# Performance work log

Hardware: AMD Instinct MI355X
Metric: run time of the kernel (lower is better)

Reference implementation:

```python
import jax, jax.numpy as jnp
import numpy as np

N, D, K = 500000, 256, 64

def setup_inputs() -> dict:
    key = jax.random.key(0)
    kq, km = jax.random.split(key)
    query = jax.random.normal(kq, (D,), dtype=jnp.float32)
    mat = jax.random.normal(km, (N, D), dtype=jnp.float32)
    return {"query": query, "mat": mat, "k": K}

def reference(query, mat, k):
    # scores = mat @ query  : [N]
    scores = jnp.einsum("nd,d->n", mat, query)
    # top-k selection over all stored vectors
    _, idx = jax.lax.top_k(scores, k)
    # gather the selected rows : [k, D]
    out = jnp.take(mat, idx, axis=0)
    # idx stands in for the metadata gather (meta[i] for i in idx)
    return out, idx
```

## Files before the change

kernel.cpp:

```cpp
#include <hip/hip_runtime.h>
#include <stdint.h>

#define DIM 256
#define TOPK 64
#define HIST_BINS 65536
#define CAP 4096

__device__ __forceinline__ uint32_t fkey(float f) {
  uint32_t u = __float_as_uint(f);
  return (u & 0x80000000u) ? ~u : (u | 0x80000000u);
}

__global__ __launch_bounds__(256) void score_kernel(
    const float* __restrict__ mat, const float* __restrict__ query,
    float* __restrict__ scores, uint32_t* __restrict__ hist,
    int* __restrict__ cnt, int n) {
  int tid = blockIdx.x * 256 + threadIdx.x;
  if (tid < HIST_BINS) hist[tid] = 0u;
  if (tid == 0) *cnt = 0;

  int wave = tid >> 6;
  int lane = threadIdx.x & 63;
  if (wave < n) {
    float4 q = ((const float4*)query)[lane];
    float4 m = ((const float4*)(mat + (size_t)wave * DIM))[lane];
    float d = m.x * q.x + m.y * q.y + m.z * q.z + m.w * q.w;
#pragma unroll
    for (int off = 32; off > 0; off >>= 1) d += __shfl_xor(d, off, 64);
    if (lane == 0) scores[wave] = d;
  }
}

__global__ __launch_bounds__(256) void hist_kernel(
    const float* __restrict__ scores, uint32_t* __restrict__ hist, int n) {
  int i = blockIdx.x * 256 + threadIdx.x;
  int stride = gridDim.x * 256;
  for (; i < n; i += stride) {
    atomicAdd(&hist[fkey(scores[i]) >> 16], 1u);
  }
}

__global__ __launch_bounds__(256) void thresh_kernel(
    const uint32_t* __restrict__ hist, int* __restrict__ tbin) {
  __shared__ uint32_t s[256];
  __shared__ int fc;
  __shared__ uint32_t above;
  int t = threadIdx.x;

  uint32_t acc = 0;
  const uint4* h4 = (const uint4*)(hist + t * 256);
  for (int j = 0; j < 64; ++j) {
    uint4 v = h4[j];
    acc += v.x + v.y + v.z + v.w;
  }
  s[t] = acc;
  __syncthreads();
  for (int off = 1; off < 256; off <<= 1) {
    uint32_t v = (t + off < 256) ? s[t + off] : 0u;
    __syncthreads();
    s[t] += v;
    __syncthreads();
  }
  if (s[t] >= TOPK && (t == 255 || s[t + 1] < TOPK)) {
    fc = t;
    above = (t == 255) ? 0u : s[t + 1];
  }
  __syncthreads();
  int c = fc;
  uint32_t a = above;
  uint32_t h = hist[c * 256 + t];
  __syncthreads();
  s[t] = h;
  __syncthreads();
  for (int off = 1; off < 256; off <<= 1) {
    uint32_t v = (t + off < 256) ? s[t + off] : 0u;
    __syncthreads();
    s[t] += v;
    __syncthreads();
  }
  if (a + s[t] >= TOPK && (t == 255 || a + s[t + 1] < TOPK)) {
    *tbin = c * 256 + t;
  }
}

__global__ __launch_bounds__(256) void collect_kernel(
    const float* __restrict__ scores, const int* __restrict__ tbin,
    int* __restrict__ cnt, unsigned long long* __restrict__ cand, int n) {
  uint32_t T = (uint32_t)(*tbin);
  int i = blockIdx.x * 256 + threadIdx.x;
  int stride = gridDim.x * 256;
  for (; i < n; i += stride) {
    uint32_t key = fkey(scores[i]);
    if ((key >> 16) >= T) {
      int pos = atomicAdd(cnt, 1);
      if (pos < CAP) {
        cand[pos] = ((unsigned long long)key << 32) | (uint32_t)(~(uint32_t)i);
      }
    }
  }
}

__global__ __launch_bounds__(256) void final_kernel(
    const unsigned long long* __restrict__ cand, const int* __restrict__ cnt,
    const float* __restrict__ mat, float* __restrict__ out) {
  __shared__ unsigned long long c[CAP];
  __shared__ int sel[TOPK];
  int t = threadIdx.x;
  int M = *cnt;
  if (M > CAP) M = CAP;

  for (int i = t; i < M; i += 256) c[i] = cand[i];
  __syncthreads();

  for (int i = t; i < M; i += 256) {
    unsigned long long mykey = c[i];
    int rank = 0;
    for (int j = 0; j < M; ++j) rank += (c[j] > mykey) ? 1 : 0;
    if (rank < TOPK) sel[rank] = (int)(~(uint32_t)(mykey & 0xFFFFFFFFull));
  }
  __syncthreads();

  if (t < TOPK) out[TOPK * DIM + t] = (float)sel[t];

  int wv = t >> 6, lane = t & 63;
  for (int r = wv; r < TOPK; r += 4) {
    size_t row = (size_t)sel[r];
    float4 v = ((const float4*)(mat + row * DIM))[lane];
    ((float4*)(out + r * DIM))[lane] = v;
  }
}

extern "C" void kernel_launch(void* const* d_in, const int* in_sizes, int n_in,
                              void* d_out, int out_size, void* d_ws, size_t ws_size,
                              hipStream_t stream) {
  const float* query = (const float*)d_in[0];
  const float* mat = (const float*)d_in[1];
  float* out = (float*)d_out;
  int n = in_sizes[1] / DIM;

  char* ws = (char*)d_ws;
  float* scores = (float*)ws;
  uint32_t* hist = (uint32_t*)(ws + (2u << 20));
  int* tbin = (int*)(ws + (2u << 20) + HIST_BINS * 4);
  int* cnt = tbin + 1;
  unsigned long long* cand =
      (unsigned long long*)(ws + (2u << 20) + HIST_BINS * 4 + 16);

  int sblocks = (n + 3) / 4;
  score_kernel<<<sblocks, 256, 0, stream>>>(mat, query, scores, hist, cnt, n);
  hist_kernel<<<512, 256, 0, stream>>>(scores, hist, n);
  thresh_kernel<<<1, 256, 0, stream>>>(hist, tbin);
  collect_kernel<<<512, 256, 0, stream>>>(scores, tbin, cnt, cand, n);
  final_kernel<<<1, 256, 0, stream>>>(cand, cnt, mat, out);
}
```

Measured before the change: 796.7 us.

## Fuse histogram into scoring, process four rows per wave, widen final kernel

The histogram atomic update moves into the scoring kernel, so scores no longer have to be re-read in a separate histogram pass. Histogram and counter zeroing move to a small separate kernel. The scoring kernel now runs as a grid-stride loop of 2048 blocks, with each wave handling four rows using 16 lanes per row and four float4 loads each. The query is kept in registers and the shuffle reduction is shorter. The single-block final selection kernel grows to 1024 threads to parallelise the rank computation and the row gather, at the cost of atomic contention on the histogram inside the bandwidth-bound scoring pass.

```diff
diff --git a/kernel.cpp b/kernel.cpp
--- a/kernel.cpp
+++ b/kernel.cpp
@@ -11,32 +11,48 @@
   return (u & 0x80000000u) ? ~u : (u | 0x80000000u);
 }
 
+__global__ __launch_bounds__(256) void zero_kernel(uint32_t* __restrict__ hist,
+                                                   int* __restrict__ cnt) {
+  int tid = blockIdx.x * 256 + threadIdx.x;
+  ((uint4*)hist)[tid] = make_uint4(0u, 0u, 0u, 0u);
+  if (tid == 0) *cnt = 0;
+}
+
 __global__ __launch_bounds__(256) void score_kernel(
     const float* __restrict__ mat, const float* __restrict__ query,
-    float* __restrict__ scores, uint32_t* __restrict__ hist,
-    int* __restrict__ cnt, int n) {
-  int tid = blockIdx.x * 256 + threadIdx.x;
-  if (tid < HIST_BINS) hist[tid] = 0u;
-  if (tid == 0) *cnt = 0;
+    float* __restrict__ scores, uint32_t* __restrict__ hist, int n) {
+  const int lane = threadIdx.x & 63;
+  const int li = lane & 15;
+  const int sub = lane >> 4;
+  const int gw = blockIdx.x * 4 + (threadIdx.x >> 6);
+  const int W = gridDim.x * 4;
 
-  int wave = tid >> 6;
-  int lane = threadIdx.x & 63;
-  if (wave < n) {
-    float4 q = ((const float4*)query)[lane];
-    float4 m = ((const float4*)(mat + (size_t)wave * DIM))[lane];
-    float d = m.x * q.x + m.y * q.y + m.z * q.z + m.w * q.w;
+  float4 q0 = ((const float4*)query)[li];
+  float4 q1 = ((const float4*)query)[li + 16];
+  float4 q2 = ((const float4*)query)[li + 32];
+  float4 q3 = ((const float4*)query)[li + 48];
+
+  int n4 = (n + 3) >> 2;
+  for (int r4 = gw; r4 < n4; r4 += W) {
+    int row = r4 * 4 + sub;
+    float d = 0.f;
+    if (row < n) {
+      const float4* m4 = (const float4*)(mat + (size_t)row * DIM);
+      float4 a = m4[li];
+      float4 b = m4[li + 16];
+      float4 c = m4[li + 32];
+      float4 e = m4[li + 48];
+      d = a.x * q0.x + a.y * q0.y + a.z * q0.z + a.w * q0.w;
+      d += b.x * q1.x + b.y * q1.y + b.z * q1.z + b.w * q1.w;
+      d += c.x * q2.x + c.y * q2.y + c.z * q2.z + c.w * q2.w;
+      d += e.x * q3.x + e.y * q3.y + e.z * q3.z + e.w * q3.w;
+    }
 #pragma unroll
-    for (int off = 32; off > 0; off >>= 1) d += __shfl_xor(d, off, 64);
-    if (lane == 0) scores[wave] = d;
-  }
-}
-
-__global__ __launch_bounds__(256) void hist_kernel(
-    const float* __restrict__ scores, uint32_t* __restrict__ hist, int n) {
-  int i = blockIdx.x * 256 + threadIdx.x;
-  int stride = gridDim.x * 256;
-  for (; i < n; i += stride) {
-    atomicAdd(&hist[fkey(scores[i]) >> 16], 1u);
+    for (int off = 8; off > 0; off >>= 1) d += __shfl_xor(d, off, 64);
+    if (li == 0 && row < n) {
+      scores[row] = d;
+      atomicAdd(&hist[fkey(d) >> 16], 1u);
+    }
   }
 }
 
@@ -100,7 +116,7 @@
   }
 }
 
-__global__ __launch_bounds__(256) void final_kernel(
+__global__ __launch_bounds__(1024) void final_kernel(
     const unsigned long long* __restrict__ cand, const int* __restrict__ cnt,
     const float* __restrict__ mat, float* __restrict__ out) {
   __shared__ unsigned long long c[CAP];
@@ -109,10 +125,10 @@
   int M = *cnt;
   if (M > CAP) M = CAP;
 
-  for (int i = t; i < M; i += 256) c[i] = cand[i];
+  for (int i = t; i < M; i += 1024) c[i] = cand[i];
   __syncthreads();
 
-  for (int i = t; i < M; i += 256) {
+  for (int i = t; i < M; i += 1024) {
     unsigned long long mykey = c[i];
     int rank = 0;
     for (int j = 0; j < M; ++j) rank += (c[j] > mykey) ? 1 : 0;
@@ -123,7 +139,7 @@
   if (t < TOPK) out[TOPK * DIM + t] = (float)sel[t];
 
   int wv = t >> 6, lane = t & 63;
-  for (int r = wv; r < TOPK; r += 4) {
+  for (int r = wv; r < TOPK; r += 16) {
     size_t row = (size_t)sel[r];
     float4 v = ((const float4*)(mat + row * DIM))[lane];
     ((float4*)(out + r * DIM))[lane] = v;
@@ -146,10 +162,9 @@
   unsigned long long* cand =
       (unsigned long long*)(ws + (2u << 20) + HIST_BINS * 4 + 16);
 
-  int sblocks = (n + 3) / 4;
-  score_kernel<<<sblocks, 256, 0, stream>>>(mat, query, scores, hist, cnt, n);
-  hist_kernel<<<512, 256, 0, stream>>>(scores, hist, n);
+  zero_kernel<<<64, 256, 0, stream>>>(hist, cnt);
+  score_kernel<<<2048, 256, 0, stream>>>(mat, query, scores, hist, n);
   thresh_kernel<<<1, 256, 0, stream>>>(hist, tbin);
   collect_kernel<<<512, 256, 0, stream>>>(scores, tbin, cnt, cand, n);
-  final_kernel<<<1, 256, 0, stream>>>(cand, cnt, mat, out);
+  final_kernel<<<1, 1024, 0, stream>>>(cand, cnt, mat, out);
 }
```

After: 765.5 us. 3.9% less time.
